# Kernel optimization log

Measured on AMD Instinct MI355X. Metric: run time of the kernel, lower is better.

Reference implementation:

```python
import jax, jax.numpy as jnp
import numpy as np

B = 1_048_576
W = 64  # hidden width
N_FREQ = 6   # 3 dims * 6 freqs * (sin,cos) = 36
K_BLOB = 4   # one-blob bins per dim


def _freq_embed(p):
    # [B,3] -> [B,36]
    freqs = 2.0 ** jnp.arange(N_FREQ, dtype=p.dtype)
    ang = jnp.pi * p[:, :, None] * freqs  # [B,3,6]
    return jnp.concatenate([jnp.sin(ang), jnp.cos(ang)], axis=-1).reshape(p.shape[0], 3 * 2 * N_FREQ)


def _sph(d):
    # unit-square parameterization of a direction, [B,3] -> [B,2]
    d = d / (jnp.linalg.norm(d, axis=-1, keepdims=True) + 1e-8)
    u = jnp.arctan2(d[:, 1], d[:, 0]) / (2.0 * jnp.pi) + 0.5
    v = jnp.arccos(jnp.clip(d[:, 2], -1.0 + 1e-6, 1.0 - 1e-6)) / jnp.pi
    return jnp.stack([u, v], axis=-1)


def _one_blob(x, k=K_BLOB):
    # x in [0,1], [B,D] -> [B,D*k] Gaussian one-blob encoding
    centers = (jnp.arange(k, dtype=x.dtype) + 0.5) / k
    sigma = 1.0 / k
    g = jnp.exp(-0.5 * ((x[..., None] - centers) / sigma) ** 2)  # [B,D,k]
    return g.reshape(x.shape[0], -1)


def _encode(p, wi, n, alpha, beta, r):
    ones = jnp.ones((p.shape[0], 2), dtype=p.dtype)
    return jnp.concatenate([
        _freq_embed(p),                      # 36
        _one_blob(_sph(wi)),                 # 8
        _one_blob(_sph(n)),                  # 8
        _one_blob(1.0 - jnp.exp(-r)),        # 4
        alpha, beta,                         # 6
        ones,                                # 2 (implicit bias)
    ], axis=-1)                              # -> [B,64]


def _mlp(x, Ws):
    h = x
    for Wk in Ws[:-1]:
        h = jax.nn.relu(h @ Wk.T)
    return h @ Ws[-1].T  # [B,3]


def setup_inputs() -> dict:
    key = jax.random.key(0)
    ks = jax.random.split(key, 13)
    p = jax.random.normal(ks[0], (B, 3), jnp.float32)
    wi = jax.random.normal(ks[1], (B, 3), jnp.float32)
    n = jax.random.normal(ks[2], (B, 3), jnp.float32)
    alpha = jax.random.uniform(ks[3], (B, 3), jnp.float32)
    beta = jax.random.uniform(ks[4], (B, 3), jnp.float32)
    r = jax.random.uniform(ks[5], (B, 1), jnp.float32)
    s = 1.0 / np.sqrt(W)
    weights = {}
    for i in range(6):
        weights[f"W{i}"] = jax.random.normal(ks[6 + i], (W, W), jnp.float32) * s
    weights["W6"] = jax.random.normal(ks[12], (3, W), jnp.float32) * s
    return dict(p=p, wi=wi, n=n, alpha=alpha, beta=beta, r=r, **weights)


def reference(p, wi, n, alpha, beta, r, W0, W1, W2, W3, W4, W5, W6):
    x = _encode(p, wi, n, alpha, beta, r)
    out = _mlp(x, [W0, W1, W2, W3, W4, W5, W6])
    return out * (alpha + beta)  # reflectance factorization
```

## Files before the change

### kernel.cpp

```cpp
#include <hip/hip_runtime.h>


typedef _Float16 f16;
typedef f16 f16x2 __attribute__((ext_vector_type(2)));
typedef f16 f16x4 __attribute__((ext_vector_type(4)));
typedef f16 f16x8 __attribute__((ext_vector_type(8)));
typedef float f32x4 __attribute__((ext_vector_type(4)));

#define MFMA32(A, B, C) __builtin_amdgcn_mfma_f32_16x16x32_f16(A, B, C, 0, 0, 0)
#define LDS_FENCE() __asm__ volatile("" ::: "memory")

static constexpr int TILES = 4;
static constexpr int WAVES = 8;
static constexpr int BLOCK = WAVES * 64;
static constexpr int SPB   = WAVES * 64;

static constexpr int    WUNITS   = 50;
static constexpr int    WCHUNKS  = WUNITS * 64;
static constexpr size_t WS_BYTES = (size_t)WCHUNKS * 16;
static constexpr int    LDS_W    = 51200;

__host__ __device__ __forceinline__ int tau(int x) {
    return (x & 32) + ((x & 7) >> 2) * 16 + ((x >> 3) & 3) * 4 + (x & 3);
}

__device__ __forceinline__ f16x2 pkh(float a, float b) {
    return __builtin_bit_cast(f16x2, __builtin_amdgcn_cvt_pkrtz(a, b));
}

__device__ __forceinline__ f16x8 pack8(const float* f) {
    f16x2 a = pkh(f[0], f[1]);
    f16x2 b = pkh(f[2], f[3]);
    f16x2 c = pkh(f[4], f[5]);
    f16x2 d = pkh(f[6], f[7]);
    f16x8 v;
    v[0] = a[0]; v[1] = a[1]; v[2] = b[0]; v[3] = b[1];
    v[4] = c[0]; v[5] = c[1]; v[6] = d[0]; v[7] = d[1];
    return v;
}

__device__ __forceinline__ f16x4 pack4(f32x4 v) {
    f16x2 a = pkh(v[0], v[1]);
    f16x2 b = pkh(v[2], v[3]);
    f16x4 r;
    r[0] = a[0]; r[1] = a[1]; r[2] = b[0]; r[3] = b[1];
    return r;
}

__device__ __forceinline__ float fast_atan2_rev(float y, float x) {
    const float ax = __builtin_fabsf(x), ay = __builtin_fabsf(y);
    const float mx = fmaxf(ax, ay), mn = fminf(ax, ay);
    const float a = mn * __builtin_amdgcn_rcpf(fmaxf(mx, 1e-30f));
    const float s = a * a;
    float r = a * (0.99997726f + s * (-0.33262347f + s * (0.19354346f +
              s * (-0.11643287f + s * (0.05265332f - s * 0.01172120f)))));
    if (ay > ax) r = 1.5707963268f - r;
    if (x < 0.0f) r = 3.1415926536f - r;
    r = (y < 0.0f) ? -r : r;
    return r * 0.15915494309189535f;
}

__device__ __forceinline__ float fast_acos(float x) {
    const float ax = __builtin_fabsf(x);
    const float t = __builtin_amdgcn_sqrtf(1.0f - ax);
    const float p = t * (1.5707288f + ax * (-0.2121144f +
                    ax * (0.0742610f - ax * 0.0187293f)));
    return (x < 0.0f) ? (3.1415926536f - p) : p;
}

__device__ __forceinline__ void blob4(float x, float* out) {
    const float dx = x - 0.125f;
    const float E0 = __expf(-8.0f * dx * dx);
    const float R  = __expf(4.0f * dx);
    const float t1 = R * 0.60653066f;
    const float t2 = R * 0.22313016f;
    const float t3 = R * 0.082084999f;
    out[0] = E0;
    out[1] = E0 * t1;
    out[2] = out[1] * t2;
    out[3] = out[2] * t3;
}

__device__ __forceinline__ f16x8 make_wchunk(
    int c, const float* __restrict__ W0, const float* __restrict__ W1,
    const float* __restrict__ W2, const float* __restrict__ W3,
    const float* __restrict__ W4, const float* __restrict__ W5,
    const float* __restrict__ W6)
{
    const int lane2 = c & 63;
    const int unit  = c >> 6;
    const int q = lane2 >> 4, m = lane2 & 15;
    f16x8 v;
    if (unit < 48) {
        const int l = unit >> 3, kt = (unit & 7) >> 2, mt = unit & 3;
        const float* Ws[6] = {W0, W1, W2, W3, W4, W5};
        const float* __restrict__ Wl = Ws[l];
#pragma unroll
        for (int j = 0; j < 8; ++j) {
            const int x = kt * 32 + q * 8 + j;
            const int src = (l == 0) ? x : tau(x);
            v[j] = (f16)Wl[(mt * 16 + m) * 64 + src];
        }
    } else {
        const int kt = unit - 48;
#pragma unroll
        for (int j = 0; j < 8; ++j) {
            const int src = tau(kt * 32 + q * 8 + j);
            v[j] = (m < 3) ? (f16)W6[m * 64 + src] : (f16)0.0f;
        }
    }
    return v;
}

__global__ __launch_bounds__(256, 1) void pack_weights_kernel(
    const float* __restrict__ W0, const float* __restrict__ W1,
    const float* __restrict__ W2, const float* __restrict__ W3,
    const float* __restrict__ W4, const float* __restrict__ W5,
    const float* __restrict__ W6, f16* __restrict__ ws)
{
    const int c = (int)blockIdx.x * 256 + threadIdx.x;
    if (c >= WCHUNKS) return;
    *(f16x8*)(ws + (size_t)c * 8) = make_wchunk(c, W0, W1, W2, W3, W4, W5, W6);
}

__device__ __forceinline__ f16x8 cat44(f16x4 a, f16x4 b) {
    return __builtin_shufflevector(a, b, 0, 1, 2, 3, 4, 5, 6, 7);
}

template<int PACKED>
__global__ __launch_bounds__(BLOCK, 4) void nrc_mlp_kernel(
    const float* __restrict__ P,  const float* __restrict__ WI,
    const float* __restrict__ NV, const float* __restrict__ AL,
    const float* __restrict__ BE, const float* __restrict__ RR,
    const f16*   __restrict__ ws,
    const float* __restrict__ W0, const float* __restrict__ W1,
    const float* __restrict__ W2, const float* __restrict__ W3,
    const float* __restrict__ W4, const float* __restrict__ W5,
    const float* __restrict__ W6, float* __restrict__ Out)
{
    __shared__ __attribute__((aligned(16))) unsigned char smem[LDS_W];

    const int tid  = threadIdx.x;
    const int lane = tid & 63;
    const int w    = tid >> 6;
    const int q    = lane >> 4;
    const int m    = lane & 15;
    unsigned char* const hb = smem + w * 2048;

    const int wave_base = (int)blockIdx.x * SPB + w * 64;

    float feat[64];
    float ab0, ab1, ab2;

    {
        const int s = wave_base + lane;

        float pv[3], wv[3], nv[3], av[3], bv[3];
#pragma unroll
        for (int d = 0; d < 3; ++d) {
            pv[d] = P [s * 3 + d];
            wv[d] = WI[s * 3 + d];
            nv[d] = NV[s * 3 + d];
            av[d] = AL[s * 3 + d];
            bv[d] = BE[s * 3 + d];
        }
        const float rv = RR[s];

#pragma unroll
        for (int d = 0; d < 3; ++d) {
            const float fr = __builtin_amdgcn_fractf(pv[d] * 0.5f);
            float sv = __builtin_amdgcn_sinf(fr);
            float cv = __builtin_amdgcn_cosf(fr);
            feat[d * 12 + 0] = sv;
            feat[d * 12 + 6] = cv;
#pragma unroll
            for (int k = 1; k < 6; ++k) {
                const float s2 = sv * sv;
                const float sc = sv * cv;
                cv = fmaf(-2.0f, s2, 1.0f);
                sv = sc + sc;
                feat[d * 12 + k]     = sv;
                feat[d * 12 + 6 + k] = cv;
            }
        }
#pragma unroll
        for (int which = 0; which < 2; ++which) {
            const float* dv = (which == 0) ? wv : nv;
            const int fo = 36 + which * 8;
            const float nr = __builtin_amdgcn_sqrtf(dv[0]*dv[0] + dv[1]*dv[1] + dv[2]*dv[2]) + 1e-8f;
            const float u  = fast_atan2_rev(dv[1], dv[0]) + 0.5f;
            float zc = dv[2] * __builtin_amdgcn_rcpf(nr);
            zc = fminf(fmaxf(zc, -1.0f + 1e-6f), 1.0f - 1e-6f);
            const float vv = fast_acos(zc) * 0.3183098861837907f;
            blob4(u,  &feat[fo]);
            blob4(vv, &feat[fo + 4]);
        }
        blob4(1.0f - __expf(-rv), &feat[52]);

        feat[56] = av[0]; feat[57] = av[1]; feat[58] = av[2];
        feat[59] = bv[0]; feat[60] = bv[1]; feat[61] = bv[2];
        feat[62] = 1.0f;  feat[63] = 1.0f;

        ab0 = av[0] + bv[0];
        ab1 = av[1] + bv[1];
        ab2 = av[2] + bv[2];
    }

    const int te = lane >> 4;
    f16x8 bf[TILES][2];
#pragma unroll
    for (int pass = 0; pass < TILES; ++pass) {
        if (te == pass) {
            unsigned char* const tb = hb + m * 128;
#pragma unroll
            for (int g = 0; g < 8; ++g) {
                const int slot0 = (4 * g + 4 * m) & 31;
                *(f16x8*)(tb + slot0 * 4) = pack8(&feat[g * 8]);
            }
        }
        LDS_FENCE();
#pragma unroll
        for (int kt = 0; kt < 2; ++kt) {
            const int s0 = (16 * kt + 4 * q + 4 * m) & 31;
            bf[pass][kt] = *(const f16x8*)(hb + m * 128 + s0 * 4);
        }
        LDS_FENCE();
    }

    __syncthreads();

#pragma unroll
    for (int i = 0; i < (WCHUNKS + BLOCK - 1) / BLOCK; ++i) {
        const int c = i * BLOCK + tid;
        if (c < WCHUNKS) {
            f16x8 v;
            if (PACKED) v = *(const f16x8*)(ws + (size_t)c * 8);
            else        v = make_wchunk(c, W0, W1, W2, W3, W4, W5, W6);
            *(f16x8*)(smem + c * 16) = v;
        }
    }
    __syncthreads();

    const f16x4 zero4 = {(f16)0.0f, (f16)0.0f, (f16)0.0f, (f16)0.0f};
    unsigned char* const wb = smem + lane * 16;

#pragma unroll
    for (int layer = 0; layer < 6; ++layer) {
        f16x8 wa[8];
#pragma unroll
        for (int f = 0; f < 8; ++f)
            wa[f] = *(const f16x8*)(wb + (layer * 8 + f) * 1024);

#pragma unroll
        for (int t = 0; t < TILES; ++t) {
            f32x4 acc[4];
#pragma unroll
            for (int mt = 0; mt < 4; ++mt) {
                f32x4 z = {0.0f, 0.0f, 0.0f, 0.0f};
                z = MFMA32(wa[mt],     bf[t][0], z);
                z = MFMA32(wa[4 + mt], bf[t][1], z);
                acc[mt] = z;
            }
            f16x4 pk[4];
#pragma unroll
            for (int mt = 0; mt < 4; ++mt)
                pk[mt] = __builtin_elementwise_max(pack4(acc[mt]), zero4);
            bf[t][0] = cat44(pk[0], pk[1]);
            bf[t][1] = cat44(pk[2], pk[3]);
        }
    }

    {
        const f16x8 w6f0 = *(const f16x8*)(wb + 48 * 1024);
        const f16x8 w6f1 = *(const f16x8*)(wb + 49 * 1024);
#pragma unroll
        for (int t = 0; t < TILES; ++t) {
            f32x4 z = {0.0f, 0.0f, 0.0f, 0.0f};
            z = MFMA32(w6f0, bf[t][0], z);
            z = MFMA32(w6f1, bf[t][1], z);
            const int src = t * 16 + m;
            const float s0 = __shfl(ab0, src);
            const float s1 = __shfl(ab1, src);
            const float s2 = __shfl(ab2, src);
            if (lane < 16) {
                const int s = wave_base + t * 16 + m;
                float* o = Out + s * 3;
                o[0] = z[0] * s0;
                o[1] = z[1] * s1;
                o[2] = z[2] * s2;
            }
        }
    }
}

extern "C" void kernel_launch(void* const* d_in, const int* in_sizes, int n_in,
                              void* d_out, int out_size, void* d_ws, size_t ws_size,
                              hipStream_t stream) {
    (void)n_in; (void)out_size;
    const float* P  = (const float*)d_in[0];
    const float* WI = (const float*)d_in[1];
    const float* NV = (const float*)d_in[2];
    const float* AL = (const float*)d_in[3];
    const float* BE = (const float*)d_in[4];
    const float* RR = (const float*)d_in[5];
    const float* W0 = (const float*)d_in[6];
    const float* W1 = (const float*)d_in[7];
    const float* W2 = (const float*)d_in[8];
    const float* W3 = (const float*)d_in[9];
    const float* W4 = (const float*)d_in[10];
    const float* W5 = (const float*)d_in[11];
    const float* W6 = (const float*)d_in[12];
    f16*   ws  = (f16*)d_ws;
    float* Out = (float*)d_out;

    const int Bn = in_sizes[0] / 3;
    const int grid = Bn / SPB;

    if (ws_size >= WS_BYTES) {
        hipLaunchKernelGGL(pack_weights_kernel, dim3((WCHUNKS + 255) / 256),
                           dim3(256), 0, stream, W0, W1, W2, W3, W4, W5, W6, ws);
        hipLaunchKernelGGL((nrc_mlp_kernel<1>), dim3(grid), dim3(BLOCK), 0, stream,
                           P, WI, NV, AL, BE, RR, ws,
                           W0, W1, W2, W3, W4, W5, W6, Out);
    } else {
        hipLaunchKernelGGL((nrc_mlp_kernel<0>), dim3(grid), dim3(BLOCK), 0, stream,
                           P, WI, NV, AL, BE, RR, ws,
                           W0, W1, W2, W3, W4, W5, W6, Out);
    }
}
```

Measured before the change: 154.3 us.

## Process four sample batches per wave and overlap next encoding with MLP layers

```diff
diff --git a/kernel.cpp b/kernel.cpp
--- a/kernel.cpp
+++ b/kernel.cpp
@@ -13,12 +13,15 @@
 static constexpr int TILES = 4;
 static constexpr int WAVES = 8;
 static constexpr int BLOCK = WAVES * 64;
-static constexpr int SPB   = WAVES * 64;
+static constexpr int NB    = 4;
+static constexpr int SPW   = 64 * NB;
+static constexpr int SPB   = WAVES * SPW;
 
 static constexpr int    WUNITS   = 50;
 static constexpr int    WCHUNKS  = WUNITS * 64;
+static constexpr int    HCHUNKS  = 48 * 64;
 static constexpr size_t WS_BYTES = (size_t)WCHUNKS * 16;
-static constexpr int    LDS_W    = 51200;
+static constexpr int    LDS_H    = 48 * 1024;
 
 __host__ __device__ __forceinline__ int tau(int x) {
     return (x & 32) + ((x & 7) >> 2) * 16 + ((x >> 3) & 3) * 4 + (x & 3);
@@ -127,8 +130,57 @@
     return __builtin_shufflevector(a, b, 0, 1, 2, 3, 4, 5, 6, 7);
 }
 
+__device__ __forceinline__ void encode64(
+    const float pv[3], const float wv[3], const float nv[3],
+    const float av[3], const float bv[3], float rv,
+    f16x8 fh[8], float& ab0, float& ab1, float& ab2)
+{
+    float feat[64];
+#pragma unroll
+    for (int d = 0; d < 3; ++d) {
+        const float fr = __builtin_amdgcn_fractf(pv[d] * 0.5f);
+        float sv = __builtin_amdgcn_sinf(fr);
+        float cv = __builtin_amdgcn_cosf(fr);
+        feat[d * 12 + 0] = sv;
+        feat[d * 12 + 6] = cv;
+#pragma unroll
+        for (int k = 1; k < 6; ++k) {
+            const float s2 = sv * sv;
+            const float sc = sv * cv;
+            cv = fmaf(-2.0f, s2, 1.0f);
+            sv = sc + sc;
+            feat[d * 12 + k]     = sv;
+            feat[d * 12 + 6 + k] = cv;
+        }
+    }
+#pragma unroll
+    for (int which = 0; which < 2; ++which) {
+        const float* dv = (which == 0) ? wv : nv;
+        const int fo = 36 + which * 8;
+        const float nr = __builtin_amdgcn_sqrtf(dv[0]*dv[0] + dv[1]*dv[1] + dv[2]*dv[2]) + 1e-8f;
+        const float u  = fast_atan2_rev(dv[1], dv[0]) + 0.5f;
+        float zc = dv[2] * __builtin_amdgcn_rcpf(nr);
+        zc = fminf(fmaxf(zc, -1.0f + 1e-6f), 1.0f - 1e-6f);
+        const float vv = fast_acos(zc) * 0.3183098861837907f;
+        blob4(u,  &feat[fo]);
+        blob4(vv, &feat[fo + 4]);
+    }
+    blob4(1.0f - __expf(-rv), &feat[52]);
+
+    feat[56] = av[0]; feat[57] = av[1]; feat[58] = av[2];
+    feat[59] = bv[0]; feat[60] = bv[1]; feat[61] = bv[2];
+    feat[62] = 1.0f;  feat[63] = 1.0f;
+
+    ab0 = av[0] + bv[0];
+    ab1 = av[1] + bv[1];
+    ab2 = av[2] + bv[2];
+
+#pragma unroll
+    for (int g = 0; g < 8; ++g) fh[g] = pack8(&feat[g * 8]);
+}
+
 template<int PACKED>
-__global__ __launch_bounds__(BLOCK, 4) void nrc_mlp_kernel(
+__global__ __launch_bounds__(BLOCK, 3) void nrc_mlp_kernel(
     const float* __restrict__ P,  const float* __restrict__ WI,
     const float* __restrict__ NV, const float* __restrict__ AL,
     const float* __restrict__ BE, const float* __restrict__ RR,
@@ -138,23 +190,47 @@
     const float* __restrict__ W4, const float* __restrict__ W5,
     const float* __restrict__ W6, float* __restrict__ Out)
 {
-    __shared__ __attribute__((aligned(16))) unsigned char smem[LDS_W];
+    __shared__ __attribute__((aligned(16))) unsigned char smem[LDS_H + WAVES * 2048];
 
     const int tid  = threadIdx.x;
     const int lane = tid & 63;
     const int w    = tid >> 6;
     const int q    = lane >> 4;
     const int m    = lane & 15;
-    unsigned char* const hb = smem + w * 2048;
-
-    const int wave_base = (int)blockIdx.x * SPB + w * 64;
-
-    float feat[64];
-    float ab0, ab1, ab2;
+    unsigned char* const hb = smem + LDS_H + w * 2048;
+
+    const int wave_samp0 = ((int)blockIdx.x * WAVES + w) * SPW;
+
+#pragma unroll
+    for (int i = 0; i < HCHUNKS / BLOCK; ++i) {
+        const int c = i * BLOCK + tid;
+        f16x8 v;
+        if (PACKED) v = *(const f16x8*)(ws + (size_t)c * 8);
+        else        v = make_wchunk(c, W0, W1, W2, W3, W4, W5, W6);
+        *(f16x8*)(smem + c * 16) = v;
+    }
+
+    f16x8 w6f0, w6f1;
+    if (PACKED) {
+        w6f0 = *(const f16x8*)(ws + 48 * 512 + (size_t)lane * 8);
+        w6f1 = *(const f16x8*)(ws + 49 * 512 + (size_t)lane * 8);
+    } else {
+        float t0[8], t1[8];
+#pragma unroll
+        for (int j = 0; j < 8; ++j) {
+            t0[j] = (m < 3) ? W6[m * 64 + tau(q * 8 + j)]      : 0.0f;
+            t1[j] = (m < 3) ? W6[m * 64 + tau(32 + q * 8 + j)] : 0.0f;
+        }
+        w6f0 = pack8(t0);
+        w6f1 = pack8(t1);
+    }
+
+    f16x8 bf[TILES][2];
+    f16x8 fh[8];
+    float abc0, abc1, abc2, abn0, abn1, abn2;
 
     {
-        const int s = wave_base + lane;
-
+        const int s = wave_samp0 + lane;
         float pv[3], wv[3], nv[3], av[3], bv[3];
 #pragma unroll
         for (int d = 0; d < 3; ++d) {
@@ -164,131 +240,132 @@
             av[d] = AL[s * 3 + d];
             bv[d] = BE[s * 3 + d];
         }
-        const float rv = RR[s];
-
-#pragma unroll
-        for (int d = 0; d < 3; ++d) {
-            const float fr = __builtin_amdgcn_fractf(pv[d] * 0.5f);
-            float sv = __builtin_amdgcn_sinf(fr);
-            float cv = __builtin_amdgcn_cosf(fr);
-            feat[d * 12 + 0] = sv;
-            feat[d * 12 + 6] = cv;
-#pragma unroll
-            for (int k = 1; k < 6; ++k) {
-                const float s2 = sv * sv;
-                const float sc = sv * cv;
-                cv = fmaf(-2.0f, s2, 1.0f);
-                sv = sc + sc;
-                feat[d * 12 + k]     = sv;
-                feat[d * 12 + 6 + k] = cv;
+        encode64(pv, wv, nv, av, bv, RR[s], fh, abn0, abn1, abn2);
+    }
+#pragma unroll
+    for (int pass = 0; pass < TILES; ++pass) {
+        if ((lane >> 4) == pass) {
+            unsigned char* const tb = hb + m * 128;
+#pragma unroll
+            for (int g = 0; g < 8; ++g)
+                *(f16x8*)(tb + ((4 * g + 4 * m) & 31) * 4) = fh[g];
+        }
+        LDS_FENCE();
+#pragma unroll
+        for (int kt = 0; kt < 2; ++kt)
+            bf[pass][kt] = *(const f16x8*)(hb + m * 128 + ((16 * kt + 4 * q + 4 * m) & 31) * 4);
+        LDS_FENCE();
+    }
+    abc0 = abn0; abc1 = abn1; abc2 = abn2;
+
+    __syncthreads();
+
+    const f16x4 zero4 = {(f16)0.0f, (f16)0.0f, (f16)0.0f, (f16)0.0f};
+
+#pragma unroll
+    for (int b = 0; b < NB; ++b) {
+        const bool more = (b + 1 < NB);
+
+        float pv[3], wv[3], nv[3], av[3], bv[3], rvv = 0.0f;
+        if (more) {
+            const int s = wave_samp0 + (b + 1) * 64 + lane;
+#pragma unroll
+            for (int d = 0; d < 3; ++d) {
+                pv[d] = P [s * 3 + d];
+                wv[d] = WI[s * 3 + d];
+                nv[d] = NV[s * 3 + d];
+                av[d] = AL[s * 3 + d];
+                bv[d] = BE[s * 3 + d];
             }
-        }
-#pragma unroll
-        for (int which = 0; which < 2; ++which) {
-            const float* dv = (which == 0) ? wv : nv;
-            const int fo = 36 + which * 8;
-            const float nr = __builtin_amdgcn_sqrtf(dv[0]*dv[0] + dv[1]*dv[1] + dv[2]*dv[2]) + 1e-8f;
-            const float u  = fast_atan2_rev(dv[1], dv[0]) + 0.5f;
-            float zc = dv[2] * __builtin_amdgcn_rcpf(nr);
-            zc = fminf(fmaxf(zc, -1.0f + 1e-6f), 1.0f - 1e-6f);
-            const float vv = fast_acos(zc) * 0.3183098861837907f;
-            blob4(u,  &feat[fo]);
-            blob4(vv, &feat[fo + 4]);
-        }
-        blob4(1.0f - __expf(-rv), &feat[52]);
-
-        feat[56] = av[0]; feat[57] = av[1]; feat[58] = av[2];
-        feat[59] = bv[0]; feat[60] = bv[1]; feat[61] = bv[2];
-        feat[62] = 1.0f;  feat[63] = 1.0f;
-
-        ab0 = av[0] + bv[0];
-        ab1 = av[1] + bv[1];
-        ab2 = av[2] + bv[2];
-    }
-
-    const int te = lane >> 4;
-    f16x8 bf[TILES][2];
-#pragma unroll
-    for (int pass = 0; pass < TILES; ++pass) {
-        if (te == pass) {
-            unsigned char* const tb = hb + m * 128;
-#pragma unroll
-            for (int g = 0; g < 8; ++g) {
-                const int slot0 = (4 * g + 4 * m) & 31;
-                *(f16x8*)(tb + slot0 * 4) = pack8(&feat[g * 8]);
+            rvv = RR[s];
+        }
+
+#pragma unroll
+        for (int layer = 0; layer < 2; ++layer) {
+            f16x8 wa[8];
+#pragma unroll
+            for (int f = 0; f < 8; ++f)
+                wa[f] = *(const f16x8*)(smem + (layer * 8 + f) * 1024 + lane * 16);
+#pragma unroll
+            for (int t = 0; t < TILES; ++t) {
+                f32x4 acc[4];
+#pragma unroll
+                for (int mt = 0; mt < 4; ++mt) {
+                    f32x4 z = {0.0f, 0.0f, 0.0f, 0.0f};
+                    z = MFMA32(wa[mt],     bf[t][0], z);
+                    z = MFMA32(wa[4 + mt], bf[t][1], z);
+                    acc[mt] = z;
+                }
+                f16x4 pk[4];
+#pragma unroll
+                for (int mt = 0; mt < 4; ++mt)
+                    pk[mt] = __builtin_elementwise_max(pack4(acc[mt]), zero4);
+                bf[t][0] = cat44(pk[0], pk[1]);
+                bf[t][1] = cat44(pk[2], pk[3]);
             }
         }
-        LDS_FENCE();
-#pragma unroll
-        for (int kt = 0; kt < 2; ++kt) {
-            const int s0 = (16 * kt + 4 * q + 4 * m) & 31;
-            bf[pass][kt] = *(const f16x8*)(hb + m * 128 + s0 * 4);
-        }
-        LDS_FENCE();
-    }
-
-    __syncthreads();
-
-#pragma unroll
-    for (int i = 0; i < (WCHUNKS + BLOCK - 1) / BLOCK; ++i) {
-        const int c = i * BLOCK + tid;
-        if (c < WCHUNKS) {
-            f16x8 v;
-            if (PACKED) v = *(const f16x8*)(ws + (size_t)c * 8);
-            else        v = make_wchunk(c, W0, W1, W2, W3, W4, W5, W6);
-            *(f16x8*)(smem + c * 16) = v;
-        }
-    }
-    __syncthreads();
-
-    const f16x4 zero4 = {(f16)0.0f, (f16)0.0f, (f16)0.0f, (f16)0.0f};
-    unsigned char* const wb = smem + lane * 16;
-
-#pragma unroll
-    for (int layer = 0; layer < 6; ++layer) {
-        f16x8 wa[8];
-#pragma unroll
-        for (int f = 0; f < 8; ++f)
-            wa[f] = *(const f16x8*)(wb + (layer * 8 + f) * 1024);
-
-#pragma unroll
-        for (int t = 0; t < TILES; ++t) {
-            f32x4 acc[4];
-#pragma unroll
-            for (int mt = 0; mt < 4; ++mt) {
-                f32x4 z = {0.0f, 0.0f, 0.0f, 0.0f};
-                z = MFMA32(wa[mt],     bf[t][0], z);
-                z = MFMA32(wa[4 + mt], bf[t][1], z);
-                acc[mt] = z;
+
+        if (more) encode64(pv, wv, nv, av, bv, rvv, fh, abn0, abn1, abn2);
+
+#pragma unroll
+        for (int layer = 2; layer < 6; ++layer) {
+            f16x8 wa[8];
+#pragma unroll
+            for (int f = 0; f < 8; ++f)
+                wa[f] = *(const f16x8*)(smem + (layer * 8 + f) * 1024 + lane * 16);
+#pragma unroll
+            for (int t = 0; t < TILES; ++t) {
+                f32x4 acc[4];
+#pragma unroll
+                for (int mt = 0; mt < 4; ++mt) {
+                    f32x4 z = {0.0f, 0.0f, 0.0f, 0.0f};
+                    z = MFMA32(wa[mt],     bf[t][0], z);
+                    z = MFMA32(wa[4 + mt], bf[t][1], z);
+                    acc[mt] = z;
+                }
+                f16x4 pk[4];
+#pragma unroll
+                for (int mt = 0; mt < 4; ++mt)
+                    pk[mt] = __builtin_elementwise_max(pack4(acc[mt]), zero4);
+                bf[t][0] = cat44(pk[0], pk[1]);
+                bf[t][1] = cat44(pk[2], pk[3]);
             }
-            f16x4 pk[4];
-#pragma unroll
-            for (int mt = 0; mt < 4; ++mt)
-                pk[mt] = __builtin_elementwise_max(pack4(acc[mt]), zero4);
-            bf[t][0] = cat44(pk[0], pk[1]);
-            bf[t][1] = cat44(pk[2], pk[3]);
-        }
-    }
-
-    {
-        const f16x8 w6f0 = *(const f16x8*)(wb + 48 * 1024);
-        const f16x8 w6f1 = *(const f16x8*)(wb + 49 * 1024);
+        }
+
 #pragma unroll
         for (int t = 0; t < TILES; ++t) {
             f32x4 z = {0.0f, 0.0f, 0.0f, 0.0f};
             z = MFMA32(w6f0, bf[t][0], z);
             z = MFMA32(w6f1, bf[t][1], z);
             const int src = t * 16 + m;
-            const float s0 = __shfl(ab0, src);
-            const float s1 = __shfl(ab1, src);
-            const float s2 = __shfl(ab2, src);
+            const float s0 = __shfl(abc0, src);
+            const float s1 = __shfl(abc1, src);
+            const float s2 = __shfl(abc2, src);
             if (lane < 16) {
-                const int s = wave_base + t * 16 + m;
+                const int s = wave_samp0 + b * 64 + t * 16 + m;
                 float* o = Out + s * 3;
                 o[0] = z[0] * s0;
                 o[1] = z[1] * s1;
                 o[2] = z[2] * s2;
             }
+        }
+
+        if (more) {
+#pragma unroll
+            for (int pass = 0; pass < TILES; ++pass) {
+                if ((lane >> 4) == pass) {
+                    unsigned char* const tb = hb + m * 128;
+#pragma unroll
+                    for (int g = 0; g < 8; ++g)
+                        *(f16x8*)(tb + ((4 * g + 4 * m) & 31) * 4) = fh[g];
+                }
+                LDS_FENCE();
+#pragma unroll
+                for (int kt = 0; kt < 2; ++kt)
+                    bf[pass][kt] = *(const f16x8*)(hb + m * 128 + ((16 * kt + 4 * q + 4 * m) & 31) * 4);
+                LDS_FENCE();
+            }
+            abc0 = abn0; abc1 = abn1; abc2 = abn2;
         }
     }
 }
```

After: 158.4 us. 1.03x slower.
